# Optimization experiments

Hardware: AMD Instinct MI355X
Metric: run time of the kernel (lower is better)

## Reference

```python
import jax, jax.numpy as jnp
import numpy as np

EMBED = 1024
HEADS = 16
HEAD_DIM = EMBED // HEADS
B, S = 2, 2048


def setup_inputs() -> dict:
    key = jax.random.key(0)
    ks = jax.random.split(key, 9)
    std = 1.0 / np.sqrt(EMBED)
    mk = lambda k: jax.random.uniform(k, (EMBED, EMBED), jnp.float32, -std, std)
    bk = lambda k: jax.random.uniform(k, (EMBED,), jnp.float32, -std, std)
    return {
        "x": jax.random.normal(ks[0], (B, S, EMBED), jnp.float32),
        "Wq": mk(ks[1]), "bq": bk(ks[2]),
        "Wk": mk(ks[3]), "bk": bk(ks[4]),
        "Wv": mk(ks[5]), "bv": bk(ks[6]),
        "Wo": mk(ks[7]), "bo": bk(ks[8]),
    }


def reference(x, Wq, bq, Wk, bk, Wv, bv, Wo, bo):
    b, s, _ = x.shape
    scale = HEAD_DIM ** -0.5
    # Linear layers: y = x @ W^T + b (torch nn.Linear convention)
    def heads(W, bias):
        y = jnp.einsum('bse,fe->bsf', x, W) + bias
        return y.reshape(b, s, HEADS, HEAD_DIM).transpose(0, 2, 1, 3)  # [b,h,s,d]
    Q, K, V = heads(Wq, bq), heads(Wk, bk), heads(Wv, bv)
    scores = jnp.einsum('bhqd,bhkd->bhqk', Q, K) * scale
    attn = jax.nn.softmax(scores, axis=-1)
    out = jnp.einsum('bhqk,bhkd->bhqd', attn, V)
    out = out.transpose(0, 2, 1, 3).reshape(b, s, EMBED)
    return jnp.einsum('bse,fe->bsf', out, Wo) + bo
```

## Files before the change

kernel.cpp:

```cpp
#include <hip/hip_runtime.h>
#include <hip/hip_bf16.h>
#include <cstddef>

#define SEQ   2048
#define EMB   1024
#define NHEAD 16
#define HDIM  64
#define BATCH 2
#define MROWS (BATCH * SEQ)
#define BH_STRIDE (SEQ * HDIM)
#define CSC_F 0.180336874f

typedef __attribute__((ext_vector_type(8))) short frag_ab;
typedef __attribute__((ext_vector_type(4))) float frag_cd;

#define GLOBAL_AS __attribute__((address_space(1)))
#define LDS_AS    __attribute__((address_space(3)))

__device__ __forceinline__ unsigned short f2bf(float f) {
    unsigned u = __float_as_uint(f);
    u += 0x7FFF + ((u >> 16) & 1);
    return (unsigned short)(u >> 16);
}
__device__ __forceinline__ unsigned short f2bf_trunc(float f) {
    return (unsigned short)(__float_as_uint(f) >> 16);
}
__device__ __forceinline__ void gld16(const unsigned short* g, unsigned short* l) {
    __builtin_amdgcn_global_load_lds((GLOBAL_AS const unsigned int*)g,
                                     (LDS_AS unsigned int*)l, 16, 0, 0);
}

__global__ __launch_bounds__(256) void cvt_all(const float* __restrict__ x,
                                               const float* __restrict__ Wq,
                                               const float* __restrict__ Wk,
                                               const float* __restrict__ Wv,
                                               unsigned short* __restrict__ xb,
                                               unsigned short* __restrict__ wqkv) {
    size_t e = ((size_t)blockIdx.x * 256 + threadIdx.x) * 8;
    const float* s;
    unsigned short* d;
    float sc = 1.0f;
    const size_t NX = (size_t)MROWS * EMB;
    const size_t NW = (size_t)EMB * EMB;
    if (e < NX) { s = x + e; d = xb + e; }
    else if (e < NX + NW)     { s = Wq + (e - NX);          d = wqkv + (e - NX); sc = CSC_F; }
    else if (e < NX + 2 * NW) { s = Wk + (e - NX - NW);     d = wqkv + (e - NX); }
    else                      { s = Wv + (e - NX - 2 * NW); d = wqkv + (e - NX); }
    float4 f0 = *(const float4*)s;
    float4 f1 = *(const float4*)(s + 4);
    ushort4 lo, hi;
    lo.x = f2bf(f0.x * sc); lo.y = f2bf(f0.y * sc); lo.z = f2bf(f0.z * sc); lo.w = f2bf(f0.w * sc);
    hi.x = f2bf(f1.x * sc); hi.y = f2bf(f1.y * sc); hi.z = f2bf(f1.z * sc); hi.w = f2bf(f1.w * sc);
    *(ushort4*)d = lo;
    *(ushort4*)(d + 4) = hi;
}

__global__ __launch_bounds__(256) void cvt_bf16(const float* __restrict__ s,
                                                unsigned short* __restrict__ d, int n) {
    int i = (blockIdx.x * 256 + threadIdx.x) * 8;
    if (i >= n) return;
    float4 f0 = *(const float4*)&s[i];
    float4 f1 = *(const float4*)&s[i + 4];
    ushort4 lo, hi;
    lo.x = f2bf(f0.x); lo.y = f2bf(f0.y); lo.z = f2bf(f0.z); lo.w = f2bf(f0.w);
    hi.x = f2bf(f1.x); hi.y = f2bf(f1.y); hi.z = f2bf(f1.z); hi.w = f2bf(f1.w);
    *(ushort4*)&d[i] = lo;
    *(ushort4*)&d[i + 4] = hi;
}

template <bool QKV>
__global__ __launch_bounds__(256, 3) void gemm128(const unsigned short* __restrict__ A,
                                                  const unsigned short* __restrict__ W0,
                                                  const unsigned short* __restrict__ W1,
                                                  const unsigned short* __restrict__ W2,
                                                  const float* __restrict__ b0,
                                                  const float* __restrict__ b1,
                                                  const float* __restrict__ b2,
                                                  void* __restrict__ o0,
                                                  void* __restrict__ o1,
                                                  void* __restrict__ o2) {
    constexpr int K = EMB;
    __shared__ __align__(16) unsigned short SB[16384];
    unsigned short* As = SB;
    unsigned short* Bs = SB + 8192;

    const int bidx = blockIdx.x;
    const int g8 = bidx & 7, t = bidx >> 3;
    const int my = g8 * 4 + (t & 3);
    const int mx = QKV ? ((t >> 2) & 7) : (t >> 2);
    const int z = QKV ? (t >> 5) : 0;

    const unsigned short* W = (z == 0) ? W0 : (z == 1) ? W1 : W2;
    const float* bias = (z == 0) ? b0 : (z == 1) ? b1 : b2;
    void* outv = (z == 0) ? o0 : (z == 1) ? o1 : o2;

    const int m0 = my * 128;
    const int n0 = mx * 128;
    const int tid = threadIdx.x;
    const int lane = tid & 63, w = tid >> 6;
    const int wr = w >> 1, wc = w & 1;
    const int lm = lane & 15, lq = lane >> 4;

    const int cs = (((tid & 7) ^ ((tid >> 3) & 7)) << 3);
    const int sx = lm & 7;

    frag_cd acc[4][4];
#pragma unroll
    for (int mt = 0; mt < 4; ++mt)
#pragma unroll
        for (int nt = 0; nt < 4; ++nt) acc[mt][nt] = (frag_cd){0.f, 0.f, 0.f, 0.f};

    for (int k0 = 0; k0 < K; k0 += 64) {
#pragma unroll
        for (int it = 0; it < 4; ++it) {
            int flat = (it * 256 + tid) * 8;
            int r = flat >> 6;
            gld16(&A[(size_t)(m0 + r) * K + k0 + cs], &As[flat]);
        }
#pragma unroll
        for (int it = 0; it < 4; ++it) {
            int flat = (it * 256 + tid) * 8;
            int r = flat >> 6;
            gld16(&W[(size_t)(n0 + r) * K + k0 + cs], &Bs[flat]);
        }
        __syncthreads();

#pragma unroll
        for (int kk = 0; kk < 2; ++kk) {
            frag_ab af[4], bf[4];
#pragma unroll
            for (int mt = 0; mt < 4; ++mt)
                af[mt] = *(const frag_ab*)&As[(wr * 64 + mt * 16 + lm) * 64
                                              + (((kk * 4 + lq) ^ sx) << 3)];
#pragma unroll
            for (int nt = 0; nt < 4; ++nt)
                bf[nt] = *(const frag_ab*)&Bs[(wc * 64 + nt * 16 + lm) * 64
                                              + (((kk * 4 + lq) ^ sx) << 3)];
#pragma unroll
            for (int mt = 0; mt < 4; ++mt)
#pragma unroll
                for (int nt = 0; nt < 4; ++nt)
                    acc[mt][nt] = __builtin_amdgcn_mfma_f32_16x16x32_bf16(
                        af[mt], bf[nt], acc[mt][nt], 0, 0, 0);
        }
        __syncthreads();
    }

    const float bscale = (QKV && z == 0) ? CSC_F : 1.0f;
    if (!QKV) {
#pragma unroll
        for (int mt = 0; mt < 4; ++mt)
#pragma unroll
            for (int nt = 0; nt < 4; ++nt) {
                int col = n0 + wc * 64 + nt * 16 + lm;
                float bv = bias[col];
#pragma unroll
                for (int r = 0; r < 4; ++r) {
                    int row = m0 + wr * 64 + mt * 16 + lq * 4 + r;
                    ((float*)outv)[(size_t)row * EMB + col] = acc[mt][nt][r] + bv;
                }
            }
    } else {
#pragma unroll
        for (int mt = 0; mt < 4; ++mt)
#pragma unroll
            for (int nt = 0; nt < 4; ++nt) {
                int col = n0 + wc * 64 + nt * 16 + lm;
                float bv = bias[col] * bscale;
#pragma unroll
                for (int r = 0; r < 4; ++r) {
                    unsigned short o = f2bf(acc[mt][nt][r] + bv);
                    int l, pos;
                    if (z < 2) {
                        l = wc * 16 + (wr * 4 + mt) * 2 + (nt >> 1);
                        pos = ((nt * 2 + (lm >> 3)) & 3) * 128 + (lq * 4 + r) * 8 + (lm & 7);
                    } else {
                        l = wc * 16 + (wr * 2 + (mt >> 1)) * 4 + nt;
                        pos = ((mt & 1) * 2 + (lq >> 1)) * 128 + lm * 8 + (lq & 1) * 4 + r;
                    }
                    SB[l * 512 + pos] = o;
                }
            }
        __syncthreads();

        unsigned short* out = (unsigned short*)outv;
        const int b = m0 >> 11;
        const int hb = n0 >> 6;
        const int sg16 = (m0 & (SEQ - 1)) >> 4;
        const int sb32 = (m0 & (SEQ - 1)) >> 5;
#pragma unroll
        for (int it = 0; it < 8; ++it) {
            int cl = it * 4 + w;
            uint4 v = *(const uint4*)&SB[cl * 512 + lane * 8];
            size_t chunk;
            if (z < 2) {
                int h = cl >> 4, sg = (cl >> 1) & 7, dh = cl & 1;
                chunk = ((size_t)(b * NHEAD + hb + h) * 128 + sg16 + sg) * 2 + dh;
            } else {
                int h = cl >> 4, sb = (cl >> 2) & 3, dq = cl & 3;
                chunk = ((size_t)(b * NHEAD + hb + h) * 64 + sb32 + sb) * 4 + dq;
            }
            *(uint4*)&out[chunk * 512 + lane * 8] = v;
        }
    }
}

#define PSTRIDE 72
__global__ __launch_bounds__(256) void attn_fused(const unsigned short* __restrict__ Q,
                                                  const unsigned short* __restrict__ Kf,
                                                  const unsigned short* __restrict__ Vf,
                                                  unsigned short* __restrict__ O) {
    const int bidx = blockIdx.x;
    const int g8 = bidx & 7, t = bidx >> 3;
    const int bh = g8 * 4 + (t & 3);
    const int qt = t >> 2;
    const int w = threadIdx.x >> 6, lane = threadIdx.x & 63;
    const int lm = lane & 15, lq = lane >> 4;

    __shared__ __align__(16) unsigned short P[4][32 * PSTRIDE];

    const unsigned short* Qb = Q + (size_t)bh * BH_STRIDE;
    const unsigned short* Kb = Kf + (size_t)bh * BH_STRIDE;
    const unsigned short* Vb = Vf + (size_t)bh * BH_STRIDE;

    const int ga = qt * 8 + w * 2;
    frag_ab qf[2][2];
#pragma unroll
    for (int qi = 0; qi < 2; ++qi) {
        qf[qi][0] = *(const frag_ab*)&Qb[(((ga + qi) * 2 + 0) * 64 + lane) * 8];
        qf[qi][1] = *(const frag_ab*)&Qb[(((ga + qi) * 2 + 1) * 64 + lane) * 8];
    }

    frag_ab vone;
#pragma unroll
    for (int j = 0; j < 8; ++j) vone[j] = (short)0x3F80;

    frag_cd oa[2][4], oc[2];
#pragma unroll
    for (int qi = 0; qi < 2; ++qi) {
        oc[qi] = (frag_cd){0.f, 0.f, 0.f, 0.f};
#pragma unroll
        for (int dt = 0; dt < 4; ++dt) oa[qi][dt] = (frag_cd){0.f, 0.f, 0.f, 0.f};
    }

    frag_ab kc[4][2], vc[2][4];
#pragma unroll
    for (int c = 0; c < 4; ++c) {
        kc[c][0] = *(const frag_ab*)&Kb[((c * 2 + 0) * 64 + lane) * 8];
        kc[c][1] = *(const frag_ab*)&Kb[((c * 2 + 1) * 64 + lane) * 8];
    }
#pragma unroll
    for (int jj = 0; jj < 2; ++jj)
#pragma unroll
        for (int dt = 0; dt < 4; ++dt)
            vc[jj][dt] = *(const frag_ab*)&Vb[((jj * 4 + dt) * 64 + lane) * 8];

    for (int j0 = 0; j0 < SEQ; j0 += 64) {
        const int jn = (j0 + 64) & (SEQ - 1);
        const int kgn = jn >> 4, jbn = jn >> 5;
        frag_ab kn[4][2], vn[2][4];
#pragma unroll
        for (int c = 0; c < 4; ++c) {
            kn[c][0] = *(const frag_ab*)&Kb[(((kgn + c) * 2 + 0) * 64 + lane) * 8];
            kn[c][1] = *(const frag_ab*)&Kb[(((kgn + c) * 2 + 1) * 64 + lane) * 8];
        }
#pragma unroll
        for (int jj = 0; jj < 2; ++jj)
#pragma unroll
            for (int dt = 0; dt < 4; ++dt)
                vn[jj][dt] = *(const frag_ab*)&Vb[(((jbn + jj) * 4 + dt) * 64 + lane) * 8];

        const frag_cd z = (frag_cd){0.f, 0.f, 0.f, 0.f};
#pragma unroll
        for (int c = 0; c < 4; ++c) {
#pragma unroll
            for (int qi = 0; qi < 2; ++qi) {
                frag_cd s = __builtin_amdgcn_mfma_f32_16x16x32_bf16(qf[qi][0], kc[c][0], z, 0, 0, 0);
                s = __builtin_amdgcn_mfma_f32_16x16x32_bf16(qf[qi][1], kc[c][1], s, 0, 0, 0);
#pragma unroll
                for (int r = 0; r < 4; ++r) {
                    float p = __builtin_amdgcn_exp2f(s[r]);
                    P[w][(qi * 16 + lq * 4 + r) * PSTRIDE + c * 16 + lm] = f2bf_trunc(p);
                }
            }
        }

        frag_ab pf[2][2];
#pragma unroll
        for (int qi = 0; qi < 2; ++qi) {
            pf[qi][0] = *(const frag_ab*)&P[w][(qi * 16 + lm) * PSTRIDE + lq * 8];
            pf[qi][1] = *(const frag_ab*)&P[w][(qi * 16 + lm) * PSTRIDE + 32 + lq * 8];
            oc[qi] = __builtin_amdgcn_mfma_f32_16x16x32_bf16(pf[qi][0], vone, oc[qi], 0, 0, 0);
            oc[qi] = __builtin_amdgcn_mfma_f32_16x16x32_bf16(pf[qi][1], vone, oc[qi], 0, 0, 0);
        }

#pragma unroll
        for (int dt = 0; dt < 4; ++dt)
#pragma unroll
            for (int qi = 0; qi < 2; ++qi) {
                oa[qi][dt] = __builtin_amdgcn_mfma_f32_16x16x32_bf16(pf[qi][0], vc[0][dt], oa[qi][dt], 0, 0, 0);
                oa[qi][dt] = __builtin_amdgcn_mfma_f32_16x16x32_bf16(pf[qi][1], vc[1][dt], oa[qi][dt], 0, 0, 0);
            }

#pragma unroll
        for (int c = 0; c < 4; ++c) { kc[c][0] = kn[c][0]; kc[c][1] = kn[c][1]; }
#pragma unroll
        for (int jj = 0; jj < 2; ++jj)
#pragma unroll
            for (int dt = 0; dt < 4; ++dt) vc[jj][dt] = vn[jj][dt];
    }

    const int b = bh >> 4, h = bh & (NHEAD - 1);
#pragma unroll
    for (int qi = 0; qi < 2; ++qi) {
        const int q0 = (ga + qi) * 16;
#pragma unroll
        for (int r = 0; r < 4; ++r) {
            float inv = 1.0f / oc[qi][r];
            int srow = q0 + lq * 4 + r;
#pragma unroll
            for (int dt = 0; dt < 4; ++dt) {
                int d = dt * 16 + lm;
                O[((size_t)(b * SEQ + srow)) * EMB + h * HDIM + d] = f2bf(oa[qi][dt][r] * inv);
            }
        }
    }
}

extern "C" void kernel_launch(void* const* d_in, const int* in_sizes, int n_in,
                              void* d_out, int out_size, void* d_ws, size_t ws_size,
                              hipStream_t stream) {
    const float* x  = (const float*)d_in[0];
    const float* Wq = (const float*)d_in[1];
    const float* bq = (const float*)d_in[2];
    const float* Wk = (const float*)d_in[3];
    const float* bk = (const float*)d_in[4];
    const float* Wv = (const float*)d_in[5];
    const float* bv = (const float*)d_in[6];
    const float* Wo = (const float*)d_in[7];
    const float* bo = (const float*)d_in[8];

    unsigned short* xb    = (unsigned short*)d_ws;
    unsigned short* q_ws  = xb + (size_t)MROWS * EMB;
    unsigned short* k_ws  = q_ws + (size_t)MROWS * EMB;
    unsigned short* vt_ws = k_ws + (size_t)MROWS * EMB;
    unsigned short* o_ws  = xb;
    unsigned short* wqkv  = (unsigned short*)d_out;
    unsigned short* wo_b  = q_ws;

    dim3 blk(256);
    cvt_all<<<dim3((MROWS * EMB + 3 * EMB * EMB) / 2048), blk, 0, stream>>>(
        x, Wq, Wk, Wv, xb, wqkv);

    gemm128<true><<<dim3(768), blk, 0, stream>>>(
        xb, wqkv, wqkv + EMB * EMB, wqkv + 2 * EMB * EMB,
        bq, bk, bv, q_ws, k_ws, vt_ws);

    attn_fused<<<dim3(512), blk, 0, stream>>>(q_ws, k_ws, vt_ws, o_ws);

    cvt_bf16<<<dim3(EMB * EMB / 2048), blk, 0, stream>>>(Wo, wo_b, EMB * EMB);
    gemm128<false><<<dim3(256), blk, 0, stream>>>(
        o_ws, wo_b, wo_b, wo_b, bo, bo, bo, d_out, d_out, d_out);
}
```

Before: 188.0 us.

## Split attention KV range across wave pairs with 64-row query tiles and LDS reduction

Each wave now handles 64 query rows (up from 32) over half of the key sequence, so every K/V fragment load feeds twice as many MFMAs. The two key halves are combined at the end through an LDS reduction of the output and row-sum accumulators. The explicit register prefetch of the next K/V tile is removed, and launch bounds ask for 2 blocks per CU. The larger per-wave accumulator set raises register pressure, and dropping the prefetch may expose global-load latency.

```diff
diff --git a/kernel.cpp b/kernel.cpp
--- a/kernel.cpp
+++ b/kernel.cpp
@@ -206,27 +206,32 @@
 }
 
 #define PSTRIDE 72
-__global__ __launch_bounds__(256) void attn_fused(const unsigned short* __restrict__ Q,
-                                                  const unsigned short* __restrict__ Kf,
-                                                  const unsigned short* __restrict__ Vf,
-                                                  unsigned short* __restrict__ O) {
+#define CSTRIDE 81
+
+__global__ __launch_bounds__(256, 2) void attn_fused(const unsigned short* __restrict__ Q,
+                                                     const unsigned short* __restrict__ Kf,
+                                                     const unsigned short* __restrict__ Vf,
+                                                     unsigned short* __restrict__ O) {
     const int bidx = blockIdx.x;
     const int g8 = bidx & 7, t = bidx >> 3;
     const int bh = g8 * 4 + (t & 3);
     const int qt = t >> 2;
     const int w = threadIdx.x >> 6, lane = threadIdx.x & 63;
     const int lm = lane & 15, lq = lane >> 4;
-
-    __shared__ __align__(16) unsigned short P[4][32 * PSTRIDE];
+    const int qs = w & 1;
+    const int kh = w >> 1;
+
+    __shared__ __align__(16) unsigned char SMEM[2 * 64 * CSTRIDE * 4 * sizeof(float) / 4];
+    unsigned short* P = (unsigned short*)SMEM;
 
     const unsigned short* Qb = Q + (size_t)bh * BH_STRIDE;
     const unsigned short* Kb = Kf + (size_t)bh * BH_STRIDE;
     const unsigned short* Vb = Vf + (size_t)bh * BH_STRIDE;
 
-    const int ga = qt * 8 + w * 2;
-    frag_ab qf[2][2];
-#pragma unroll
-    for (int qi = 0; qi < 2; ++qi) {
+    const int ga = qt * 8 + qs * 4;
+    frag_ab qf[4][2];
+#pragma unroll
+    for (int qi = 0; qi < 4; ++qi) {
         qf[qi][0] = *(const frag_ab*)&Qb[(((ga + qi) * 2 + 0) * 64 + lane) * 8];
         qf[qi][1] = *(const frag_ab*)&Qb[(((ga + qi) * 2 + 1) * 64 + lane) * 8];
     }
@@ -235,93 +240,106 @@
 #pragma unroll
     for (int j = 0; j < 8; ++j) vone[j] = (short)0x3F80;
 
-    frag_cd oa[2][4], oc[2];
-#pragma unroll
-    for (int qi = 0; qi < 2; ++qi) {
+    frag_cd oa[4][4], oc[4];
+#pragma unroll
+    for (int qi = 0; qi < 4; ++qi) {
         oc[qi] = (frag_cd){0.f, 0.f, 0.f, 0.f};
 #pragma unroll
         for (int dt = 0; dt < 4; ++dt) oa[qi][dt] = (frag_cd){0.f, 0.f, 0.f, 0.f};
     }
 
-    frag_ab kc[4][2], vc[2][4];
-#pragma unroll
-    for (int c = 0; c < 4; ++c) {
-        kc[c][0] = *(const frag_ab*)&Kb[((c * 2 + 0) * 64 + lane) * 8];
-        kc[c][1] = *(const frag_ab*)&Kb[((c * 2 + 1) * 64 + lane) * 8];
-    }
-#pragma unroll
-    for (int jj = 0; jj < 2; ++jj)
-#pragma unroll
-        for (int dt = 0; dt < 4; ++dt)
-            vc[jj][dt] = *(const frag_ab*)&Vb[((jj * 4 + dt) * 64 + lane) * 8];
-
-    for (int j0 = 0; j0 < SEQ; j0 += 64) {
-        const int jn = (j0 + 64) & (SEQ - 1);
-        const int kgn = jn >> 4, jbn = jn >> 5;
-        frag_ab kn[4][2], vn[2][4];
+    unsigned short* Pw = &P[w * (64 * PSTRIDE)];
+    const frag_cd z = (frag_cd){0.f, 0.f, 0.f, 0.f};
+
+    const int j_base = kh * (SEQ / 2);
+    for (int jj = 0; jj < SEQ / 2; jj += 64) {
+        const int j = j_base + jj;
+        const int kg = j >> 4, jb = j >> 5;
+
+        frag_ab kc[4][2], vc[2][4];
 #pragma unroll
         for (int c = 0; c < 4; ++c) {
-            kn[c][0] = *(const frag_ab*)&Kb[(((kgn + c) * 2 + 0) * 64 + lane) * 8];
-            kn[c][1] = *(const frag_ab*)&Kb[(((kgn + c) * 2 + 1) * 64 + lane) * 8];
-        }
-#pragma unroll
-        for (int jj = 0; jj < 2; ++jj)
+            kc[c][0] = *(const frag_ab*)&Kb[(((kg + c) * 2 + 0) * 64 + lane) * 8];
+            kc[c][1] = *(const frag_ab*)&Kb[(((kg + c) * 2 + 1) * 64 + lane) * 8];
+        }
+#pragma unroll
+        for (int j2 = 0; j2 < 2; ++j2)
 #pragma unroll
             for (int dt = 0; dt < 4; ++dt)
-                vn[jj][dt] = *(const frag_ab*)&Vb[(((jbn + jj) * 4 + dt) * 64 + lane) * 8];
-
-        const frag_cd z = (frag_cd){0.f, 0.f, 0.f, 0.f};
+                vc[j2][dt] = *(const frag_ab*)&Vb[(((jb + j2) * 4 + dt) * 64 + lane) * 8];
+
 #pragma unroll
         for (int c = 0; c < 4; ++c) {
 #pragma unroll
-            for (int qi = 0; qi < 2; ++qi) {
-                frag_cd s = __builtin_amdgcn_mfma_f32_16x16x32_bf16(qf[qi][0], kc[c][0], z, 0, 0, 0);
-                s = __builtin_amdgcn_mfma_f32_16x16x32_bf16(qf[qi][1], kc[c][1], s, 0, 0, 0);
+            for (int qi = 0; qi < 4; ++qi) {
+                frag_cd sc = __builtin_amdgcn_mfma_f32_16x16x32_bf16(qf[qi][0], kc[c][0], z, 0, 0, 0);
+                sc = __builtin_amdgcn_mfma_f32_16x16x32_bf16(qf[qi][1], kc[c][1], sc, 0, 0, 0);
 #pragma unroll
                 for (int r = 0; r < 4; ++r) {
-                    float p = __builtin_amdgcn_exp2f(s[r]);
-                    P[w][(qi * 16 + lq * 4 + r) * PSTRIDE + c * 16 + lm] = f2bf_trunc(p);
+                    float p = __builtin_amdgcn_exp2f(sc[r]);
+                    Pw[(qi * 16 + lq * 4 + r) * PSTRIDE + c * 16 + lm] = f2bf_trunc(p);
                 }
             }
         }
 
-        frag_ab pf[2][2];
-#pragma unroll
-        for (int qi = 0; qi < 2; ++qi) {
-            pf[qi][0] = *(const frag_ab*)&P[w][(qi * 16 + lm) * PSTRIDE + lq * 8];
-            pf[qi][1] = *(const frag_ab*)&P[w][(qi * 16 + lm) * PSTRIDE + 32 + lq * 8];
-            oc[qi] = __builtin_amdgcn_mfma_f32_16x16x32_bf16(pf[qi][0], vone, oc[qi], 0, 0, 0);
-            oc[qi] = __builtin_amdgcn_mfma_f32_16x16x32_bf16(pf[qi][1], vone, oc[qi], 0, 0, 0);
-        }
-
-#pragma unroll
-        for (int dt = 0; dt < 4; ++dt)
-#pragma unroll
-            for (int qi = 0; qi < 2; ++qi) {
-                oa[qi][dt] = __builtin_amdgcn_mfma_f32_16x16x32_bf16(pf[qi][0], vc[0][dt], oa[qi][dt], 0, 0, 0);
-                oa[qi][dt] = __builtin_amdgcn_mfma_f32_16x16x32_bf16(pf[qi][1], vc[1][dt], oa[qi][dt], 0, 0, 0);
-            }
-
-#pragma unroll
-        for (int c = 0; c < 4; ++c) { kc[c][0] = kn[c][0]; kc[c][1] = kn[c][1]; }
-#pragma unroll
-        for (int jj = 0; jj < 2; ++jj)
-#pragma unroll
-            for (int dt = 0; dt < 4; ++dt) vc[jj][dt] = vn[jj][dt];
-    }
-
-    const int b = bh >> 4, h = bh & (NHEAD - 1);
-#pragma unroll
-    for (int qi = 0; qi < 2; ++qi) {
-        const int q0 = (ga + qi) * 16;
-#pragma unroll
-        for (int r = 0; r < 4; ++r) {
-            float inv = 1.0f / oc[qi][r];
-            int srow = q0 + lq * 4 + r;
+#pragma unroll
+        for (int qi = 0; qi < 4; ++qi) {
+            frag_ab pf0 = *(const frag_ab*)&Pw[(qi * 16 + lm) * PSTRIDE + lq * 8];
+            frag_ab pf1 = *(const frag_ab*)&Pw[(qi * 16 + lm) * PSTRIDE + 32 + lq * 8];
+            oc[qi] = __builtin_amdgcn_mfma_f32_16x16x32_bf16(pf0, vone, oc[qi], 0, 0, 0);
+            oc[qi] = __builtin_amdgcn_mfma_f32_16x16x32_bf16(pf1, vone, oc[qi], 0, 0, 0);
 #pragma unroll
             for (int dt = 0; dt < 4; ++dt) {
-                int d = dt * 16 + lm;
-                O[((size_t)(b * SEQ + srow)) * EMB + h * HDIM + d] = f2bf(oa[qi][dt][r] * inv);
+                oa[qi][dt] = __builtin_amdgcn_mfma_f32_16x16x32_bf16(pf0, vc[0][dt], oa[qi][dt], 0, 0, 0);
+                oa[qi][dt] = __builtin_amdgcn_mfma_f32_16x16x32_bf16(pf1, vc[1][dt], oa[qi][dt], 0, 0, 0);
+            }
+        }
+    }
+
+    __syncthreads();
+    float* C = (float*)SMEM;
+    if (w >= 2) {
+        float* dst = C + (size_t)(w - 2) * (64 * CSTRIDE) + lane * CSTRIDE;
+        int idx = 0;
+#pragma unroll
+        for (int qi = 0; qi < 4; ++qi)
+#pragma unroll
+            for (int dt = 0; dt < 4; ++dt)
+#pragma unroll
+                for (int r = 0; r < 4; ++r) dst[idx++] = oa[qi][dt][r];
+#pragma unroll
+        for (int qi = 0; qi < 4; ++qi)
+#pragma unroll
+            for (int r = 0; r < 4; ++r) dst[idx++] = oc[qi][r];
+    }
+    __syncthreads();
+    if (w < 2) {
+        const float* src = C + (size_t)w * (64 * CSTRIDE) + lane * CSTRIDE;
+        int idx = 0;
+#pragma unroll
+        for (int qi = 0; qi < 4; ++qi)
+#pragma unroll
+            for (int dt = 0; dt < 4; ++dt)
+#pragma unroll
+                for (int r = 0; r < 4; ++r) oa[qi][dt][r] += src[idx++];
+#pragma unroll
+        for (int qi = 0; qi < 4; ++qi)
+#pragma unroll
+            for (int r = 0; r < 4; ++r) oc[qi][r] += src[idx++];
+
+        const int b = bh >> 4, h = bh & (NHEAD - 1);
+#pragma unroll
+        for (int qi = 0; qi < 4; ++qi) {
+            const int q0 = (ga + qi) * 16;
+#pragma unroll
+            for (int r = 0; r < 4; ++r) {
+                float inv = 1.0f / oc[qi][r];
+                int srow = q0 + lq * 4 + r;
+#pragma unroll
+                for (int dt = 0; dt < 4; ++dt) {
+                    int d = dt * 16 + lm;
+                    O[((size_t)(b * SEQ + srow)) * EMB + h * HDIM + d] = f2bf(oa[qi][dt][r] * inv);
+                }
             }
         }
     }
```

New measurement: 179.9 us. -4.3%, faster.
